# Kernel tuning notes

Measured on AMD Instinct MI355X. Metric: run time of the kernel, lower is better.

Reference implementation:

```python
import jax, jax.numpy as jnp
from jax import lax
import numpy as np

B, L = 256, 4096
H, RL, RH = 128, 2, 32   # num_hiddens, residual layers, residual hiddens
K, D = 512, 64           # codebook size, embedding dim
CC = 0.25                # commitment cost


def conv1d(x, w, b=None, stride=1, pad=0, circular=False):
    # x: (N,C,L), w: (O,I,k)
    if circular and pad > 0:
        x = jnp.pad(x, ((0, 0), (0, 0), (pad, pad)), mode='wrap')
        pad = 0
    y = lax.conv_general_dilated(x, w, (stride,), [(pad, pad)],
                                 dimension_numbers=('NCH', 'OIH', 'NCH'))
    return y if b is None else y + b[None, :, None]


def convt1d(x, w, b):
    # PyTorch ConvTranspose1d(k=4, s=2, p=1); w: (I,O,4). out_len = 2*L.
    wt = jnp.flip(jnp.swapaxes(w, 0, 1), -1)  # (O,I,4)
    y = lax.conv_general_dilated(x, wt, (1,), [(2, 2)], lhs_dilation=(2,),
                                 dimension_numbers=('NCH', 'OIH', 'NCH'))
    return y + b[None, :, None]


def res_stack(x, w1s, w2s):
    for i in range(w1s.shape[0]):
        h = conv1d(jax.nn.relu(x), w1s[i], None, 1, 1, circular=True)
        h = conv1d(jax.nn.relu(h), w2s[i], None, 1, 0)
        x = x + h
    return jax.nn.relu(x)


def setup_inputs() -> dict:
    key = jax.random.key(0)
    ks = iter(jax.random.split(key, 64))

    def w(*shape):
        fan_in = int(np.prod(shape[1:]))
        return jax.random.normal(next(ks), shape, jnp.float32) / np.sqrt(fan_in)

    def bias(n):
        return jax.random.uniform(next(ks), (n,), jnp.float32, -0.05, 0.05)

    inp = {'x': jax.random.normal(next(ks), (B, 1, L), jnp.float32)}
    # Encoder
    inp['enc_c1_w'] = w(H // 2, 1, 4);      inp['enc_c1_b'] = bias(H // 2)
    inp['enc_c2_w'] = w(H, H // 2, 4);      inp['enc_c2_b'] = bias(H)
    inp['enc_c3_w'] = w(H, H, 4);           inp['enc_c3_b'] = bias(H)
    inp['enc_c4_w'] = w(H, H, 4);           inp['enc_c4_b'] = bias(H)
    inp['enc_cf_w'] = w(H, H, 3);           inp['enc_cf_b'] = bias(H)
    inp['enc_res_w1'] = w(RL, RH, H, 3)
    inp['enc_res_w2'] = w(RL, H, RH, 1)
    # pre-VQ 1x1 conv
    inp['prevq_w'] = w(D, H, 1);            inp['prevq_b'] = bias(D)
    # codebook: uniform(-1/K, 1/K) as in source
    inp['emb'] = jax.random.uniform(next(ks), (K, D), jnp.float32, -1.0 / K, 1.0 / K)
    # Decoder
    inp['dec_init_w'] = w(H, D, 3);         inp['dec_init_b'] = bias(H)
    inp['dec_res_w1'] = w(RL, RH, H, 3)
    inp['dec_res_w2'] = w(RL, H, RH, 1)
    inp['ct0_w'] = w(H, H, 4);              inp['ct0_b'] = bias(H)
    inp['ct1_w'] = w(H, H, 4);              inp['ct1_b'] = bias(H)
    inp['ct2_w'] = w(H, H // 2, 4);         inp['ct2_b'] = bias(H // 2)
    inp['ct3_w'] = w(H // 2, 1, 4);         inp['ct3_b'] = bias(1)
    return inp


def _forward(x, enc_c1_w, enc_c1_b, enc_c2_w, enc_c2_b, enc_c3_w, enc_c3_b,
             enc_c4_w, enc_c4_b, enc_cf_w, enc_cf_b, enc_res_w1, enc_res_w2,
             prevq_w, prevq_b, emb, dec_init_w, dec_init_b, dec_res_w1,
             dec_res_w2, ct0_w, ct0_b, ct1_w, ct1_b, ct2_w, ct2_b, ct3_w, ct3_b):
    sg = lax.stop_gradient
    relu = jax.nn.relu
    # ---- Encoder (circular padding) ----
    z = relu(conv1d(x, enc_c1_w, enc_c1_b, 2, 1, circular=True))
    z = relu(conv1d(z, enc_c2_w, enc_c2_b, 2, 1, circular=True))
    z = relu(conv1d(z, enc_c3_w, enc_c3_b, 2, 1, circular=True))
    z = relu(conv1d(z, enc_c4_w, enc_c4_b, 2, 1, circular=True))
    z = conv1d(z, enc_cf_w, enc_cf_b, 1, 1, circular=True)
    z = res_stack(z, enc_res_w1, enc_res_w2)
    z = conv1d(z, prevq_w, prevq_b, 1, 0)        # (B, D, T)
    # ---- Vector quantizer ----
    z_t = jnp.transpose(z, (0, 2, 1))            # (B, T, D)
    flat = z_t.reshape(-1, D)                    # (BT, D)
    dist = (jnp.sum(flat ** 2, axis=1, keepdims=True)
            + jnp.sum(emb ** 2, axis=1)
            - 2.0 * flat @ emb.T)                # (BT, K)
    idx = jnp.argmin(dist, axis=1)               # (BT,)
    enc = jax.nn.one_hot(idx, K, dtype=flat.dtype)
    q = (enc @ emb).reshape(z_t.shape)           # (B, T, D)
    e_loss = jnp.mean((sg(q) - z_t) ** 2)
    q_loss = jnp.mean((q - sg(z_t)) ** 2)
    loss = q_loss + CC * e_loss
    q_st = z_t + sg(q - z_t)                     # straight-through
    avg = jnp.mean(enc, axis=0)
    perplexity = jnp.exp(-jnp.sum(avg * jnp.log(avg + 1e-10)))
    quantized = jnp.transpose(q_st, (0, 2, 1))   # (B, D, T)
    # ---- Decoder ----
    h = conv1d(quantized, dec_init_w, dec_init_b, 1, 1)
    h = res_stack(h, dec_res_w1, dec_res_w2)
    h = relu(convt1d(h, ct0_w, ct0_b))
    h = relu(convt1d(h, ct1_w, ct1_b))
    h = relu(convt1d(h, ct2_w, ct2_b))
    x_recon = convt1d(h, ct3_w, ct3_b)           # (B, 1, L)
    return loss, x_recon, perplexity


def reference(x, enc_c1_w, enc_c1_b, enc_c2_w, enc_c2_b, enc_c3_w, enc_c3_b,
              enc_c4_w, enc_c4_b, enc_cf_w, enc_cf_b, enc_res_w1, enc_res_w2,
              prevq_w, prevq_b, emb, dec_init_w, dec_init_b, dec_res_w1,
              dec_res_w2, ct0_w, ct0_b, ct1_w, ct1_b, ct2_w, ct2_b, ct3_w, ct3_b):
    return _forward(x, enc_c1_w, enc_c1_b, enc_c2_w, enc_c2_b, enc_c3_w,
                    enc_c3_b, enc_c4_w, enc_c4_b, enc_cf_w, enc_cf_b,
                    enc_res_w1, enc_res_w2, prevq_w, prevq_b, emb,
                    dec_init_w, dec_init_b, dec_res_w1, dec_res_w2,
                    ct0_w, ct0_b, ct1_w, ct1_b, ct2_w, ct2_b, ct3_w, ct3_b)
```

## Files before the change

### kernel.cpp

```cpp
#include <hip/hip_runtime.h>

#define DEVI __device__ __forceinline__

typedef __bf16 bf16x8 __attribute__((ext_vector_type(8)));
typedef float f32x4 __attribute__((ext_vector_type(4)));

DEVI ushort f2b(float f) {
  uint b = __float_as_uint(f);
  uint r = (b + 0x7FFFu + ((b >> 16) & 1u)) >> 16;
  return (ushort)r;
}
DEVI float b2f(ushort u) { return __uint_as_float(((uint)u) << 16); }

struct PrepArgs {
  int nw;
  int tot[20];
  const float* src[20];
  ushort* dst[20];
  int ci[20], co[20], sco[20], sci[20], sk[20];
};

__global__ __launch_bounds__(256)
void prep_all(PrepArgs a, int total) {
  int i = blockIdx.x * 256 + threadIdx.x;
  if (i >= total) return;
  int w = 0;
  while (i >= a.tot[w]) { i -= a.tot[w]; ++w; }
  const int li = i;
  const int CI = a.ci[w];
  int ciX = i % CI;
  int rest = i / CI;
  int coX = rest % a.co[w];
  int k = rest / a.co[w];
  a.dst[w][li] = f2b(a.src[w][coX * a.sco[w] + ciX * a.sci[w] + k * a.sk[w]]);
}

__global__ __launch_bounds__(256)
void enc1_bf(const float* __restrict__ x, const float* __restrict__ w1,
             const float* __restrict__ b1, ushort* __restrict__ out) {
  int i = blockIdx.x * 256 + threadIdx.x;
  int t = i & 2047, n = i >> 11;
  const float* xb = x + ((size_t)n << 12);
  int p = 2 * t - 1;
  float x0 = xb[(p + 4096) & 4095];
  float x1 = xb[(p + 4097) & 4095];
  float x2 = xb[(p + 4098) & 4095];
  float x3 = xb[(p + 4099) & 4095];
  uint ow[32];
  #pragma unroll
  for (int c2 = 0; c2 < 32; ++c2) {
    float4 wa = *reinterpret_cast<const float4*>(w1 + 8 * c2);
    float4 wb = *reinterpret_cast<const float4*>(w1 + 8 * c2 + 4);
    float s0 = fmaf(wa.x, x0, fmaf(wa.y, x1, fmaf(wa.z, x2, fmaf(wa.w, x3, b1[2 * c2]))));
    float s1 = fmaf(wb.x, x0, fmaf(wb.y, x1, fmaf(wb.z, x2, fmaf(wb.w, x3, b1[2 * c2 + 1]))));
    ow[c2] = (uint)f2b(fmaxf(s0, 0.0f)) | ((uint)f2b(fmaxf(s1, 0.0f)) << 16);
  }
  uint4* op = reinterpret_cast<uint4*>(out + ((size_t)i << 6));
  #pragma unroll
  for (int q = 0; q < 8; ++q)
    op[q] = uint4{ow[4 * q], ow[4 * q + 1], ow[4 * q + 2], ow[4 * q + 3]};
}

template<int CI, int CO, int K, int S, bool CIRC, bool GATHER>
__global__ __launch_bounds__(256)
void conv_mfma(const ushort* __restrict__ in, const ushort* __restrict__ wb,
               const float* __restrict__ bias, const ushort* __restrict__ resid,
               ushort* __restrict__ out, const int* __restrict__ gidx,
               int Tin, int in_relu, int out_relu) {
  constexpr int PAD = (K > 1) ? 1 : 0;
  constexpr int NT = 4;
  constexpr int TT = NT * 16;
  constexpr int SPAN = S * (TT - 1) + K;
  constexpr int CIG = CI / 8;
  constexpr int COT = CO / 16;
  constexpr int WCOT = (COT + 3) / 4;
  constexpr int WAVES_CO = COT / WCOT;
  constexpr int WAVES_T = 4 / WAVES_CO;
  constexpr int WTT = NT / WAVES_T;
  static_assert(CI % 32 == 0, "");

  __shared__ __align__(16) ushort xs[SPAN * CI];

  const int Tout = Tin / S;
  const int tilesPerB = Tout / TT;
  const int n = blockIdx.x / tilesPerB;
  const int t0 = (blockIdx.x % tilesPerB) * TT;
  const int tid = threadIdx.x;
  const int wid = tid >> 6, lane = tid & 63;
  const int l15 = lane & 15, l4 = lane >> 4;

  const int t_in0 = S * t0 - PAD;
  const ushort* inb = GATHER ? in : in + (size_t)n * Tin * CI;
  for (int i = tid; i < SPAN * CIG; i += 256) {
    int t = i / CIG, g = i - (i / CIG) * CIG;
    int tg = t_in0 + t;
    uint4 v;
    if (CIRC) {
      tg = (tg < 0) ? tg + Tin : (tg >= Tin ? tg - Tin : tg);
      v = *reinterpret_cast<const uint4*>(inb + (size_t)tg * CI + g * 8);
    } else if (GATHER) {
      if ((unsigned)tg < (unsigned)Tin) {
        int id = gidx[n * Tin + tg];
        v = *reinterpret_cast<const uint4*>(inb + (size_t)id * CI + g * 8);
      } else
        v = uint4{0, 0, 0, 0};
    } else {
      if ((unsigned)tg < (unsigned)Tin)
        v = *reinterpret_cast<const uint4*>(inb + (size_t)tg * CI + g * 8);
      else
        v = uint4{0, 0, 0, 0};
    }
    if (in_relu) {
      ushort* pv = reinterpret_cast<ushort*>(&v);
      #pragma unroll
      for (int e = 0; e < 8; ++e) pv[e] = (pv[e] & 0x8000) ? 0 : pv[e];
    }
    *reinterpret_cast<uint4*>(&xs[t * CI + ((g ^ (t & (CIG - 1))) * 8)]) = v;
  }
  __syncthreads();

  const int wco = wid % WAVES_CO;
  const int wt = wid / WAVES_CO;
  const int co_base = wco * WCOT * 16;
  const int t_base = wt * WTT * 16;

  f32x4 acc[WTT][WCOT] = {};

  for (int cc = 0; cc < CI / 32; ++cc) {
    #pragma unroll
    for (int k = 0; k < K; ++k) {
      bf16x8 bfr[WCOT];
      #pragma unroll
      for (int c = 0; c < WCOT; ++c) {
        const ushort* wp = wb + (size_t)((k * CO + co_base + c * 16 + l15)) * CI + cc * 32 + l4 * 8;
        bfr[c] = __builtin_bit_cast(bf16x8, *reinterpret_cast<const uint4*>(wp));
      }
      #pragma unroll
      for (int tt2 = 0; tt2 < WTT; ++tt2) {
        int trow = S * (t_base + tt2 * 16 + l15) + k;
        int g = cc * 4 + l4;
        bf16x8 afr = __builtin_bit_cast(bf16x8, *reinterpret_cast<const uint4*>(
            &xs[trow * CI + ((g ^ (trow & (CIG - 1))) * 8)]));
        #pragma unroll
        for (int c = 0; c < WCOT; ++c)
          acc[tt2][c] = __builtin_amdgcn_mfma_f32_16x16x32_bf16(afr, bfr[c], acc[tt2][c], 0, 0, 0);
      }
    }
  }

  float bv[WCOT];
  #pragma unroll
  for (int c = 0; c < WCOT; ++c)
    bv[c] = bias ? bias[co_base + c * 16 + l15] : 0.0f;
  ushort* outb = out + (size_t)n * Tout * CO;
  const ushort* resb = resid ? resid + (size_t)n * Tout * CO : nullptr;
  #pragma unroll
  for (int tt2 = 0; tt2 < WTT; ++tt2)
    #pragma unroll
    for (int c = 0; c < WCOT; ++c)
      #pragma unroll
      for (int r = 0; r < 4; ++r) {
        int t = t0 + t_base + tt2 * 16 + 4 * l4 + r;
        int co = co_base + c * 16 + l15;
        float v = acc[tt2][c][r] + bv[c];
        if (resb) v += b2f(resb[(size_t)t * CO + co]);
        if (out_relu) v = fmaxf(v, 0.0f);
        outb[(size_t)t * CO + co] = f2b(v);
      }
}

__global__ __launch_bounds__(256)
void res_mfma(const ushort* __restrict__ in, const ushort* __restrict__ wb1,
              const ushort* __restrict__ wb2, ushort* __restrict__ out) {
  constexpr int CI = 128, CIG = 16;
  constexpr int TT = 64, SPAN = 66, Tin = 256;
  __shared__ __align__(16) ushort xs[SPAN * CI];
  __shared__ __align__(16) ushort hs[TT][40];
  const int n = blockIdx.x >> 2;
  const int t0 = (blockIdx.x & 3) * TT;
  const int tid = threadIdx.x;
  const int wid = tid >> 6, lane = tid & 63;
  const int l15 = lane & 15, l4 = lane >> 4;
  const int t_in0 = t0 - 1;
  const ushort* inb = in + (size_t)n * Tin * CI;

  for (int i = tid; i < SPAN * CIG; i += 256) {
    int t = i >> 4, g = i & 15;
    int tg = t_in0 + t;
    tg = (tg < 0) ? tg + Tin : (tg >= Tin ? tg - Tin : tg);
    uint4 v = *reinterpret_cast<const uint4*>(inb + (size_t)tg * CI + g * 8);
    ushort* pv = reinterpret_cast<ushort*>(&v);
    #pragma unroll
    for (int e = 0; e < 8; ++e) pv[e] = (pv[e] & 0x8000) ? 0 : pv[e];
    *reinterpret_cast<uint4*>(&xs[t * CI + ((g ^ (t & 15)) * 8)]) = v;
  }
  __syncthreads();

  {
    f32x4 acc[2] = {};
    for (int cc = 0; cc < 4; ++cc)
      #pragma unroll
      for (int k = 0; k < 3; ++k) {
        bf16x8 bfr[2];
        #pragma unroll
        for (int c = 0; c < 2; ++c)
          bfr[c] = __builtin_bit_cast(bf16x8, *reinterpret_cast<const uint4*>(
              wb1 + (size_t)((k * 32 + c * 16 + l15)) * CI + cc * 32 + l4 * 8));
        int trow = wid * 16 + l15 + k;
        int g = cc * 4 + l4;
        bf16x8 afr = __builtin_bit_cast(bf16x8, *reinterpret_cast<const uint4*>(
            &xs[trow * CI + ((g ^ (trow & 15)) * 8)]));
        acc[0] = __builtin_amdgcn_mfma_f32_16x16x32_bf16(afr, bfr[0], acc[0], 0, 0, 0);
        acc[1] = __builtin_amdgcn_mfma_f32_16x16x32_bf16(afr, bfr[1], acc[1], 0, 0, 0);
      }
    #pragma unroll
    for (int c = 0; c < 2; ++c)
      #pragma unroll
      for (int r = 0; r < 4; ++r) {
        float v = acc[c][r];
        hs[wid * 16 + l4 * 4 + r][c * 16 + l15] = (v > 0.0f) ? f2b(v) : (ushort)0;
      }
  }
  __syncthreads();

  {
    bf16x8 afr = *reinterpret_cast<const bf16x8*>(&hs[wid * 16 + l15][l4 * 8]);
    f32x4 acc[8];
    #pragma unroll
    for (int c = 0; c < 8; ++c) {
      bf16x8 bfr = __builtin_bit_cast(bf16x8, *reinterpret_cast<const uint4*>(
          wb2 + (size_t)(c * 16 + l15) * 32 + l4 * 8));
      f32x4 z = {};
      acc[c] = __builtin_amdgcn_mfma_f32_16x16x32_bf16(afr, bfr, z, 0, 0, 0);
    }
    ushort* outb = out + (size_t)n * Tin * CI;
    #pragma unroll
    for (int c = 0; c < 8; ++c)
      #pragma unroll
      for (int r = 0; r < 4; ++r) {
        int t = t0 + wid * 16 + l4 * 4 + r;
        int co = c * 16 + l15;
        float v = acc[c][r] + b2f(inb[(size_t)t * CI + co]);
        outb[(size_t)t * CI + co] = f2b(v);
      }
  }
}

template<int CO>
__global__ __launch_bounds__(256)
void convt_mfma(const ushort* __restrict__ in, const ushort* __restrict__ wb,
                const float* __restrict__ bias, ushort* __restrict__ out,
                int Tin, int in_relu, int out_relu) {
  constexpr int CI = 128, CIG = 16;
  constexpr int NT = 4, TT = 64;
  constexpr int SPAN = TT + 2;
  constexpr int COT = CO / 16;
  constexpr int WCOT = (COT + 3) / 4;
  constexpr int WAVES_CO = COT / WCOT;
  constexpr int WTT = NT;

  __shared__ __align__(16) ushort xs[SPAN * CI];

  const int Tout = 2 * Tin;
  const int tilesPerB = Tin / TT;
  const int n = blockIdx.x / tilesPerB;
  const int tp0 = (blockIdx.x % tilesPerB) * TT;
  const int tid = threadIdx.x;
  const int wid = tid >> 6, lane = tid & 63;
  const int l15 = lane & 15, l4 = lane >> 4;

  const int t_in0 = tp0 - 1;
  const ushort* inb = in + (size_t)n * Tin * CI;
  for (int i = tid; i < SPAN * CIG; i += 256) {
    int t = i >> 4, g = i & 15;
    int tg = t_in0 + t;
    uint4 v;
    if ((unsigned)tg < (unsigned)Tin)
      v = *reinterpret_cast<const uint4*>(inb + (size_t)tg * CI + g * 8);
    else
      v = uint4{0, 0, 0, 0};
    if (in_relu) {
      ushort* pv = reinterpret_cast<ushort*>(&v);
      #pragma unroll
      for (int e = 0; e < 8; ++e) pv[e] = (pv[e] & 0x8000) ? 0 : pv[e];
    }
    *reinterpret_cast<uint4*>(&xs[t * CI + ((g ^ (t & 15)) * 8)]) = v;
  }
  __syncthreads();

  const int wco = wid % WAVES_CO;
  const int co_base = wco * WCOT * 16;

  f32x4 accE[WTT][WCOT] = {};
  f32x4 accO[WTT][WCOT] = {};

  for (int cc = 0; cc < 4; ++cc) {
    bf16x8 bk[4][WCOT];
    #pragma unroll
    for (int k = 0; k < 4; ++k)
      #pragma unroll
      for (int c = 0; c < WCOT; ++c) {
        const ushort* wp = wb + (size_t)((k * CO + co_base + c * 16 + l15)) * CI + cc * 32 + l4 * 8;
        bk[k][c] = __builtin_bit_cast(bf16x8, *reinterpret_cast<const uint4*>(wp));
      }
    #pragma unroll
    for (int tt2 = 0; tt2 < WTT; ++tt2) {
      int lt = tt2 * 16 + l15 + 1;
      int g = cc * 4 + l4;
      bf16x8 a0 = __builtin_bit_cast(bf16x8, *reinterpret_cast<const uint4*>(
          &xs[lt * CI + ((g ^ (lt & 15)) * 8)]));
      bf16x8 am = __builtin_bit_cast(bf16x8, *reinterpret_cast<const uint4*>(
          &xs[(lt - 1) * CI + ((g ^ ((lt - 1) & 15)) * 8)]));
      bf16x8 ap = __builtin_bit_cast(bf16x8, *reinterpret_cast<const uint4*>(
          &xs[(lt + 1) * CI + ((g ^ ((lt + 1) & 15)) * 8)]));
      #pragma unroll
      for (int c = 0; c < WCOT; ++c) {
        accE[tt2][c] = __builtin_amdgcn_mfma_f32_16x16x32_bf16(a0, bk[1][c], accE[tt2][c], 0, 0, 0);
        accE[tt2][c] = __builtin_amdgcn_mfma_f32_16x16x32_bf16(am, bk[3][c], accE[tt2][c], 0, 0, 0);
        accO[tt2][c] = __builtin_amdgcn_mfma_f32_16x16x32_bf16(ap, bk[0][c], accO[tt2][c], 0, 0, 0);
        accO[tt2][c] = __builtin_amdgcn_mfma_f32_16x16x32_bf16(a0, bk[2][c], accO[tt2][c], 0, 0, 0);
      }
    }
  }

  float bv[WCOT];
  #pragma unroll
  for (int c = 0; c < WCOT; ++c) bv[c] = bias[co_base + c * 16 + l15];
  ushort* outb = out + (size_t)n * Tout * CO;
  #pragma unroll
  for (int tt2 = 0; tt2 < WTT; ++tt2)
    #pragma unroll
    for (int c = 0; c < WCOT; ++c)
      #pragma unroll
      for (int r = 0; r < 4; ++r) {
        int tp = tp0 + tt2 * 16 + 4 * l4 + r;
        int co = co_base + c * 16 + l15;
        float vE = accE[tt2][c][r] + bv[c];
        float vO = accO[tt2][c][r] + bv[c];
        if (out_relu) { vE = fmaxf(vE, 0.0f); vO = fmaxf(vO, 0.0f); }
        outb[(size_t)(2 * tp) * CO + co] = f2b(vE);
        outb[(size_t)(2 * tp + 1) * CO + co] = f2b(vO);
      }
}

__global__ __launch_bounds__(256)
void ct3_bf(const ushort* __restrict__ in, const float* __restrict__ w3,
            const float* __restrict__ b3, float* __restrict__ out) {
  constexpr int SPAN = 130;
  __shared__ __align__(16) ushort ys[SPAN * 64];
  const int n = blockIdx.x >> 4;
  const int ot0 = (blockIdx.x & 15) << 8;
  const int tid = threadIdx.x;
  const int t_in0 = (ot0 >> 1) - 1;
  const ushort* inb = in + (size_t)n * 2048 * 64;
  for (int i = tid; i < SPAN * 8; i += 256) {
    int t = i >> 3, g = i & 7;
    int tg = t_in0 + t;
    uint4 v;
    if ((unsigned)tg < 2048u)
      v = *reinterpret_cast<const uint4*>(inb + (size_t)tg * 64 + g * 8);
    else
      v = uint4{0, 0, 0, 0};
    *reinterpret_cast<uint4*>(&ys[t * 64 + ((g ^ (t & 7)) * 8)]) = v;
  }
  __syncthreads();
  const int ot = ot0 + tid;
  const int odd = ot & 1;
  const int it_a = odd ? ((ot + 1) >> 1) : (ot >> 1);
  const int it_b = odd ? ((ot - 1) >> 1) : (ot / 2 - 1);
  const int ka = odd ? 0 : 1;
  const int kb = odd ? 2 : 3;
  const int lt_a = it_a - t_in0, lt_b = it_b - t_in0;
  float s = b3[0];
  #pragma unroll
  for (int g = 0; g < 8; ++g) {
    uint4 va = *reinterpret_cast<const uint4*>(&ys[lt_a * 64 + ((g ^ (lt_a & 7)) * 8)]);
    uint4 vb = *reinterpret_cast<const uint4*>(&ys[lt_b * 64 + ((g ^ (lt_b & 7)) * 8)]);
    const ushort* pa = reinterpret_cast<const ushort*>(&va);
    const ushort* pb = reinterpret_cast<const ushort*>(&vb);
    #pragma unroll
    for (int e = 0; e < 8; ++e) {
      int ci = g * 8 + e;
      s = fmaf(w3[ci * 4 + ka], b2f(pa[e]), s);
      s = fmaf(w3[ci * 4 + kb], b2f(pb[e]), s);
    }
  }
  out[(size_t)n * 4096 + ot] = s;
}

__global__ void ee_kernel(const float* __restrict__ emb, float* __restrict__ ee) {
  int c = blockIdx.x * 256 + threadIdx.x;
  if (c >= 512) return;
  float s = 0.0f;
  #pragma unroll
  for (int d = 0; d < 64; ++d) { float v = emb[c * 64 + d]; s = fmaf(v, v, s); }
  ee[c] = s;
}

__global__ __launch_bounds__(256)
void vq_mfma(const ushort* __restrict__ zt, const ushort* __restrict__ embb,
             const float* __restrict__ ee, int* __restrict__ idx,
             int* __restrict__ hist, float* __restrict__ loss_accum) {
  __shared__ __align__(16) ushort es[512 * 64];
  __shared__ float eel[512];
  __shared__ int lhist[512];
  const int tid = threadIdx.x;
  const int wid = tid >> 6, lane = tid & 63;
  const int l15 = lane & 15, l4 = lane >> 4;

  for (int i = tid; i < 512 * 8; i += 256) {
    int c = i >> 3, g = i & 7;
    reinterpret_cast<uint4*>(es)[c * 8 + (g ^ (c & 7))] =
        reinterpret_cast<const uint4*>(embb)[i];
  }
  for (int i = tid; i < 512; i += 256) { eel[i] = ee[i]; lhist[i] = 0; }
  __syncthreads();

  const int rb = blockIdx.x * 256 + wid * 64;
  bf16x8 bz[4][2];
  float zz[4], best[4];
  int bi[4];
  #pragma unroll
  for (int rt = 0; rt < 4; ++rt) {
    const int r = rb + rt * 16 + l15;
    uint4 v0 = *reinterpret_cast<const uint4*>(zt + (size_t)r * 64 + l4 * 8);
    uint4 v1 = *reinterpret_cast<const uint4*>(zt + (size_t)r * 64 + 32 + l4 * 8);
    bz[rt][0] = __builtin_bit_cast(bf16x8, v0);
    bz[rt][1] = __builtin_bit_cast(bf16x8, v1);
    float s = 0.0f;
    const ushort* p0 = reinterpret_cast<const ushort*>(&v0);
    const ushort* p1 = reinterpret_cast<const ushort*>(&v1);
    #pragma unroll
    for (int e = 0; e < 8; ++e) {
      float f0 = b2f(p0[e]), f1 = b2f(p1[e]);
      s = fmaf(f0, f0, fmaf(f1, f1, s));
    }
    s += __shfl_xor(s, 16);
    s += __shfl_xor(s, 32);
    zz[rt] = s;
    best[rt] = 3.4e38f;
    bi[rt] = 0;
  }

  for (int ct = 0; ct < 32; ++ct) {
    const int c = ct * 16 + l15;
    bf16x8 a0 = __builtin_bit_cast(bf16x8, reinterpret_cast<const uint4*>(es)[
        c * 8 + (l4 ^ (c & 7))]);
    bf16x8 a1 = __builtin_bit_cast(bf16x8, reinterpret_cast<const uint4*>(es)[
        c * 8 + ((4 | l4) ^ (c & 7))]);
    #pragma unroll
    for (int rt = 0; rt < 4; ++rt) {
      f32x4 acc = {};
      acc = __builtin_amdgcn_mfma_f32_16x16x32_bf16(a0, bz[rt][0], acc, 0, 0, 0);
      acc = __builtin_amdgcn_mfma_f32_16x16x32_bf16(a1, bz[rt][1], acc, 0, 0, 0);
      #pragma unroll
      for (int rr = 0; rr < 4; ++rr) {
        int code = ct * 16 + l4 * 4 + rr;
        float d = eel[code] - 2.0f * acc[rr];
        if (d < best[rt] || (d == best[rt] && code < bi[rt])) { best[rt] = d; bi[rt] = code; }
      }
    }
  }
  float vsum = 0.0f;
  #pragma unroll
  for (int rt = 0; rt < 4; ++rt) {
    #pragma unroll
    for (int m = 16; m <= 32; m <<= 1) {
      float ob = __shfl_xor(best[rt], m);
      int oi = __shfl_xor(bi[rt], m);
      if (ob < best[rt] || (ob == best[rt] && oi < bi[rt])) { best[rt] = ob; bi[rt] = oi; }
    }
    if (l4 == 0) {
      idx[rb + rt * 16 + l15] = bi[rt];
      atomicAdd(&lhist[bi[rt]], 1);
      vsum += zz[rt] + best[rt];
    }
  }
  #pragma unroll
  for (int m = 1; m < 64; m <<= 1) vsum += __shfl_xor(vsum, m);
  if (lane == 0) atomicAdd(loss_accum, vsum);
  __syncthreads();
  for (int i = tid; i < 512; i += 256)
    if (lhist[i]) atomicAdd(&hist[i], lhist[i]);
}

__global__ __launch_bounds__(512)
void finalize(const int* __restrict__ hist, const float* __restrict__ loss_accum,
              float* __restrict__ out) {
  __shared__ float red[8];
  int tid = threadIdx.x;
  float avg = (float)hist[tid] * (1.0f / 65536.0f);
  float v = avg * logf(avg + 1e-10f);
  for (int off = 32; off > 0; off >>= 1) v += __shfl_down(v, off);
  if ((tid & 63) == 0) red[tid >> 6] = v;
  __syncthreads();
  if (tid == 0) {
    float s = 0.0f;
    for (int i = 0; i < 8; ++i) s += red[i];
    out[1048577] = expf(-s);
    out[0] = 1.25f * loss_accum[0] * (1.0f / (65536.0f * 64.0f));
  }
}

extern "C" void kernel_launch(void* const* d_in, const int* in_sizes, int n_in,
                              void* d_out, int out_size, void* d_ws, size_t ws_size,
                              hipStream_t stream) {
  (void)in_sizes; (void)n_in; (void)out_size; (void)ws_size;
  const float* x    = (const float*)d_in[0];
  const float* c1w  = (const float*)d_in[1];
  const float* c1b  = (const float*)d_in[2];
  const float* c2w  = (const float*)d_in[3];
  const float* c2b  = (const float*)d_in[4];
  const float* c3w  = (const float*)d_in[5];
  const float* c3b  = (const float*)d_in[6];
  const float* c4w  = (const float*)d_in[7];
  const float* c4b  = (const float*)d_in[8];
  const float* cfw  = (const float*)d_in[9];
  const float* cfb  = (const float*)d_in[10];
  const float* erw1 = (const float*)d_in[11];
  const float* erw2 = (const float*)d_in[12];
  const float* pqw  = (const float*)d_in[13];
  const float* pqb  = (const float*)d_in[14];
  const float* emb  = (const float*)d_in[15];
  const float* diw  = (const float*)d_in[16];
  const float* dib  = (const float*)d_in[17];
  const float* drw1 = (const float*)d_in[18];
  const float* drw2 = (const float*)d_in[19];
  const float* t0w  = (const float*)d_in[20];
  const float* t0b  = (const float*)d_in[21];
  const float* t1w  = (const float*)d_in[22];
  const float* t1b  = (const float*)d_in[23];
  const float* t2w  = (const float*)d_in[24];
  const float* t2b  = (const float*)d_in[25];
  const float* t3w  = (const float*)d_in[26];
  const float* t3b  = (const float*)d_in[27];

  char* wsb = (char*)d_ws;
  ushort* R0 = (ushort*)wsb;
  ushort* R1 = (ushort*)(wsb + 67108864);
  ushort* R2 = (ushort*)(wsb + 134217728);
  ushort* R3 = (ushort*)(wsb + 0);
  ushort* R4 = (ushort*)(wsb + 16777216);
  ushort* R6 = (ushort*)(wsb + 37748736);
  ushort* WPu = (ushort*)(wsb + 167772160);
  ushort* wb_e2 = WPu + 0;
  ushort* wb_e3 = WPu + 32768;
  ushort* wb_e4 = WPu + 98304;
  ushort* wb_cf = WPu + 163840;
  ushort* wb_r1a = WPu + 212992;
  ushort* wb_r1b = WPu + 225280;
  ushort* wb_r2a = WPu + 237568;
  ushort* wb_r2b = WPu + 241664;
  ushort* wb_pq = WPu + 245760;
  ushort* wb_di = WPu + 253952;
  ushort* wb_d1a = WPu + 278528;
  ushort* wb_d1b = WPu + 290816;
  ushort* wb_d2a = WPu + 303104;
  ushort* wb_d2b = WPu + 307200;
  ushort* wb_t0 = WPu + 311296;
  ushort* wb_t1 = WPu + 376832;
  ushort* wb_t2 = WPu + 442368;
  ushort* wb_emb = WPu + 475136;
  char* fp = wsb + 167772160 + 1048576;
  float* eeb   = (float*)fp;
  int*   idxb  = (int*)(fp + 2048);
  int*   histb = (int*)(fp + 2048 + 262144);
  float* lossb = (float*)(fp + 2048 + 262144 + 2048);
  float* outp  = (float*)d_out;

  hipMemsetAsync(histb, 0, 512 * sizeof(int), stream);
  hipMemsetAsync(lossb, 0, sizeof(float), stream);

  PrepArgs pa{};
  int nw = 0, total = 0;
  auto addw = [&](const float* src, ushort* dst, int CO, int CI, int K,
                  int sco, int sci, int sk) {
    pa.tot[nw] = K * CO * CI; pa.src[nw] = src; pa.dst[nw] = dst;
    pa.ci[nw] = CI; pa.co[nw] = CO; pa.sco[nw] = sco; pa.sci[nw] = sci; pa.sk[nw] = sk;
    total += pa.tot[nw]; ++nw;
  };
  addw(c2w, wb_e2, 128, 64, 4, 256, 4, 1);
  addw(c3w, wb_e3, 128, 128, 4, 512, 4, 1);
  addw(c4w, wb_e4, 128, 128, 4, 512, 4, 1);
  addw(cfw, wb_cf, 128, 128, 3, 384, 3, 1);
  addw(erw1, wb_r1a, 32, 128, 3, 384, 3, 1);
  addw(erw1 + 12288, wb_r1b, 32, 128, 3, 384, 3, 1);
  addw(erw2, wb_r2a, 128, 32, 1, 32, 1, 1);
  addw(erw2 + 4096, wb_r2b, 128, 32, 1, 32, 1, 1);
  addw(pqw, wb_pq, 64, 128, 1, 128, 1, 1);
  addw(diw, wb_di, 128, 64, 3, 192, 3, 1);
  addw(drw1, wb_d1a, 32, 128, 3, 384, 3, 1);
  addw(drw1 + 12288, wb_d1b, 32, 128, 3, 384, 3, 1);
  addw(drw2, wb_d2a, 128, 32, 1, 32, 1, 1);
  addw(drw2 + 4096, wb_d2b, 128, 32, 1, 32, 1, 1);
  addw(t0w, wb_t0, 128, 128, 4, 4, 512, 1);
  addw(t1w, wb_t1, 128, 128, 4, 4, 512, 1);
  addw(t2w, wb_t2, 64, 128, 4, 4, 256, 1);
  addw(emb, wb_emb, 512, 64, 1, 64, 1, 1);
  pa.nw = nw;
  prep_all<<<(total + 255) / 256, 256, 0, stream>>>(pa, total);
  ee_kernel<<<2, 256, 0, stream>>>(emb, eeb);

  enc1_bf<<<2048, 256, 0, stream>>>(x, c1w, c1b, R0);
  conv_mfma<64, 128, 4, 2, true, false><<<4096, 256, 0, stream>>>(R0, wb_e2, c2b, nullptr, R1, nullptr, 2048, 0, 1);
  conv_mfma<128, 128, 4, 2, true, false><<<2048, 256, 0, stream>>>(R1, wb_e3, c3b, nullptr, R2, nullptr, 1024, 0, 1);
  conv_mfma<128, 128, 4, 2, true, false><<<1024, 256, 0, stream>>>(R2, wb_e4, c4b, nullptr, R3, nullptr, 512, 0, 1);
  conv_mfma<128, 128, 3, 1, true, false><<<1024, 256, 0, stream>>>(R3, wb_cf, cfb, nullptr, R4, nullptr, 256, 0, 0);
  res_mfma<<<1024, 256, 0, stream>>>(R4, wb_r1a, wb_r2a, R3);
  res_mfma<<<1024, 256, 0, stream>>>(R3, wb_r1b, wb_r2b, R4);
  conv_mfma<128, 64, 1, 1, false, false><<<1024, 256, 0, stream>>>(R4, wb_pq, pqb, nullptr, R6, nullptr, 256, 1, 0);
  vq_mfma<<<256, 256, 0, stream>>>(R6, wb_emb, eeb, idxb, histb, lossb);
  finalize<<<1, 512, 0, stream>>>(histb, lossb, outp);
  conv_mfma<64, 128, 3, 1, false, true><<<1024, 256, 0, stream>>>(wb_emb, wb_di, dib, nullptr, R3, idxb, 256, 0, 0);
  res_mfma<<<1024, 256, 0, stream>>>(R3, wb_d1a, wb_d2a, R4);
  res_mfma<<<1024, 256, 0, stream>>>(R4, wb_d1b, wb_d2b, R3);
  convt_mfma<128><<<1024, 256, 0, stream>>>(R3, wb_t0, t0b, R2, 256, 1, 1);
  convt_mfma<128><<<2048, 256, 0, stream>>>(R2, wb_t1, t1b, R0, 512, 0, 1);
  convt_mfma<64><<<4096, 256, 0, stream>>>(R0, wb_t2, t2b, R1, 1024, 0, 1);
  ct3_bf<<<4096, 256, 0, stream>>>(R1, t3w, t3b, outp + 1);
}
```

Measured before the change: 463.6 us.

## Fuse enc conv1 into conv2 and convT2 into convT3, retune tile shapes

Encoder conv1 (1→64 channels) is now computed on the fly in shared memory inside a new MFMA conv2 kernel, so the large 64-channel bf16 intermediate is never written to or read from HBM. In the same way, the last two transposed convolutions are fused: the convT2 output tile stays in LDS, including halo rows computed by extra MFMAs, and feeds the scalar convT3 directly. conv_mfma gains NT and WAVES_CO template parameters so the stride-1 layers use larger time tiles with half the blocks. It also hoists all K weight fragments per channel chunk and uses a stride-aware LDS swizzle to cut bank conflicts. The trade-offs are redundant recomputation of halo rows and higher register and LDS use per block.

```diff
diff --git a/kernel.cpp b/kernel.cpp
--- a/kernel.cpp
+++ b/kernel.cpp
@@ -35,49 +35,22 @@
   a.dst[w][li] = f2b(a.src[w][coX * a.sco[w] + ciX * a.sci[w] + k * a.sk[w]]);
 }
 
-__global__ __launch_bounds__(256)
-void enc1_bf(const float* __restrict__ x, const float* __restrict__ w1,
-             const float* __restrict__ b1, ushort* __restrict__ out) {
-  int i = blockIdx.x * 256 + threadIdx.x;
-  int t = i & 2047, n = i >> 11;
-  const float* xb = x + ((size_t)n << 12);
-  int p = 2 * t - 1;
-  float x0 = xb[(p + 4096) & 4095];
-  float x1 = xb[(p + 4097) & 4095];
-  float x2 = xb[(p + 4098) & 4095];
-  float x3 = xb[(p + 4099) & 4095];
-  uint ow[32];
-  #pragma unroll
-  for (int c2 = 0; c2 < 32; ++c2) {
-    float4 wa = *reinterpret_cast<const float4*>(w1 + 8 * c2);
-    float4 wb = *reinterpret_cast<const float4*>(w1 + 8 * c2 + 4);
-    float s0 = fmaf(wa.x, x0, fmaf(wa.y, x1, fmaf(wa.z, x2, fmaf(wa.w, x3, b1[2 * c2]))));
-    float s1 = fmaf(wb.x, x0, fmaf(wb.y, x1, fmaf(wb.z, x2, fmaf(wb.w, x3, b1[2 * c2 + 1]))));
-    ow[c2] = (uint)f2b(fmaxf(s0, 0.0f)) | ((uint)f2b(fmaxf(s1, 0.0f)) << 16);
-  }
-  uint4* op = reinterpret_cast<uint4*>(out + ((size_t)i << 6));
-  #pragma unroll
-  for (int q = 0; q < 8; ++q)
-    op[q] = uint4{ow[4 * q], ow[4 * q + 1], ow[4 * q + 2], ow[4 * q + 3]};
-}
-
-template<int CI, int CO, int K, int S, bool CIRC, bool GATHER>
+template<int CI, int CO, int K, int S, bool CIRC, bool GATHER, int NT, int WAVES_CO>
 __global__ __launch_bounds__(256)
 void conv_mfma(const ushort* __restrict__ in, const ushort* __restrict__ wb,
                const float* __restrict__ bias, const ushort* __restrict__ resid,
                ushort* __restrict__ out, const int* __restrict__ gidx,
                int Tin, int in_relu, int out_relu) {
   constexpr int PAD = (K > 1) ? 1 : 0;
-  constexpr int NT = 4;
   constexpr int TT = NT * 16;
   constexpr int SPAN = S * (TT - 1) + K;
   constexpr int CIG = CI / 8;
   constexpr int COT = CO / 16;
-  constexpr int WCOT = (COT + 3) / 4;
-  constexpr int WAVES_CO = COT / WCOT;
+  constexpr int WCOT = COT / WAVES_CO;
   constexpr int WAVES_T = 4 / WAVES_CO;
   constexpr int WTT = NT / WAVES_T;
-  static_assert(CI % 32 == 0, "");
+  constexpr int KSH = (S == 2) ? 1 : 0;
+  static_assert(CI % 32 == 0 && COT % WAVES_CO == 0 && NT % WAVES_T == 0, "");
 
   __shared__ __align__(16) ushort xs[SPAN * CI];
 
@@ -115,7 +88,7 @@
       #pragma unroll
       for (int e = 0; e < 8; ++e) pv[e] = (pv[e] & 0x8000) ? 0 : pv[e];
     }
-    *reinterpret_cast<uint4*>(&xs[t * CI + ((g ^ (t & (CIG - 1))) * 8)]) = v;
+    *reinterpret_cast<uint4*>(&xs[t * CI + ((g ^ ((t >> KSH) & (CIG - 1))) * 8)]) = v;
   }
   __syncthreads();
 
@@ -127,23 +100,24 @@
   f32x4 acc[WTT][WCOT] = {};
 
   for (int cc = 0; cc < CI / 32; ++cc) {
+    bf16x8 bk[K][WCOT];
+    #pragma unroll
+    for (int k = 0; k < K; ++k)
+      #pragma unroll
+      for (int c = 0; c < WCOT; ++c)
+        bk[k][c] = __builtin_bit_cast(bf16x8, *reinterpret_cast<const uint4*>(
+            wb + (size_t)((k * CO + co_base + c * 16 + l15)) * CI + cc * 32 + l4 * 8));
     #pragma unroll
     for (int k = 0; k < K; ++k) {
-      bf16x8 bfr[WCOT];
-      #pragma unroll
-      for (int c = 0; c < WCOT; ++c) {
-        const ushort* wp = wb + (size_t)((k * CO + co_base + c * 16 + l15)) * CI + cc * 32 + l4 * 8;
-        bfr[c] = __builtin_bit_cast(bf16x8, *reinterpret_cast<const uint4*>(wp));
-      }
       #pragma unroll
       for (int tt2 = 0; tt2 < WTT; ++tt2) {
         int trow = S * (t_base + tt2 * 16 + l15) + k;
         int g = cc * 4 + l4;
         bf16x8 afr = __builtin_bit_cast(bf16x8, *reinterpret_cast<const uint4*>(
-            &xs[trow * CI + ((g ^ (trow & (CIG - 1))) * 8)]));
+            &xs[trow * CI + ((g ^ ((trow >> KSH) & (CIG - 1))) * 8)]));
         #pragma unroll
         for (int c = 0; c < WCOT; ++c)
-          acc[tt2][c] = __builtin_amdgcn_mfma_f32_16x16x32_bf16(afr, bfr[c], acc[tt2][c], 0, 0, 0);
+          acc[tt2][c] = __builtin_amdgcn_mfma_f32_16x16x32_bf16(afr, bk[k][c], acc[tt2][c], 0, 0, 0);
       }
     }
   }
@@ -166,6 +140,91 @@
         if (resb) v += b2f(resb[(size_t)t * CO + co]);
         if (out_relu) v = fmaxf(v, 0.0f);
         outb[(size_t)t * CO + co] = f2b(v);
+      }
+}
+
+__global__ __launch_bounds__(256)
+void enc12_mfma(const float* __restrict__ x, const float* __restrict__ w1,
+                const float* __restrict__ b1, const ushort* __restrict__ wb,
+                const float* __restrict__ b2, ushort* __restrict__ out) {
+  constexpr int CI = 64, CO = 128, K = 4, NT = 8;
+  constexpr int TT = 128, SPAN = 2 * 127 + 4;
+  constexpr int CIG = 8, WCOT = 4, WTT = 4;
+  __shared__ __align__(16) ushort xs[SPAN * CI];
+  __shared__ float xl[520];
+
+  const int n = blockIdx.x >> 3;
+  const int t0 = (blockIdx.x & 7) * TT;
+  const int tid = threadIdx.x;
+  const int wid = tid >> 6, lane = tid & 63;
+  const int l15 = lane & 15, l4 = lane >> 4;
+  const int t_in0 = 2 * t0 - 1;
+  const int xw0 = 2 * t_in0 - 1;
+  const float* xb = x + ((size_t)n << 12);
+
+  for (int j = tid; j < 518; j += 256)
+    xl[j] = xb[(xw0 + j + 8192) & 4095];
+  __syncthreads();
+
+  for (int i = tid; i < SPAN * CIG; i += 256) {
+    int t = i >> 3, g = i & 7;
+    float xv0 = xl[2 * t], xv1 = xl[2 * t + 1], xv2 = xl[2 * t + 2], xv3 = xl[2 * t + 3];
+    uint pack[4];
+    #pragma unroll
+    for (int h = 0; h < 4; ++h) {
+      int c0 = g * 8 + 2 * h;
+      float4 wa = *reinterpret_cast<const float4*>(w1 + 4 * c0);
+      float4 wc = *reinterpret_cast<const float4*>(w1 + 4 * c0 + 4);
+      float s0 = fmaf(wa.x, xv0, fmaf(wa.y, xv1, fmaf(wa.z, xv2, fmaf(wa.w, xv3, b1[c0]))));
+      float s1 = fmaf(wc.x, xv0, fmaf(wc.y, xv1, fmaf(wc.z, xv2, fmaf(wc.w, xv3, b1[c0 + 1]))));
+      pack[h] = (uint)f2b(fmaxf(s0, 0.0f)) | ((uint)f2b(fmaxf(s1, 0.0f)) << 16);
+    }
+    *reinterpret_cast<uint4*>(&xs[t * CI + ((g ^ ((t >> 1) & 7)) * 8)]) =
+        uint4{pack[0], pack[1], pack[2], pack[3]};
+  }
+  __syncthreads();
+
+  const int wco = wid & 1;
+  const int wt = wid >> 1;
+  const int co_base = wco * 64;
+  const int t_base = wt * 64;
+
+  f32x4 acc[WTT][WCOT] = {};
+  for (int cc = 0; cc < 2; ++cc) {
+    bf16x8 bk[K][WCOT];
+    #pragma unroll
+    for (int k = 0; k < K; ++k)
+      #pragma unroll
+      for (int c = 0; c < WCOT; ++c)
+        bk[k][c] = __builtin_bit_cast(bf16x8, *reinterpret_cast<const uint4*>(
+            wb + (size_t)((k * CO + co_base + c * 16 + l15)) * CI + cc * 32 + l4 * 8));
+    #pragma unroll
+    for (int k = 0; k < K; ++k) {
+      #pragma unroll
+      for (int tt2 = 0; tt2 < WTT; ++tt2) {
+        int trow = 2 * (t_base + tt2 * 16 + l15) + k;
+        int g = cc * 4 + l4;
+        bf16x8 afr = __builtin_bit_cast(bf16x8, *reinterpret_cast<const uint4*>(
+            &xs[trow * CI + ((g ^ ((trow >> 1) & 7)) * 8)]));
+        #pragma unroll
+        for (int c = 0; c < WCOT; ++c)
+          acc[tt2][c] = __builtin_amdgcn_mfma_f32_16x16x32_bf16(afr, bk[k][c], acc[tt2][c], 0, 0, 0);
+      }
+    }
+  }
+  float bv[WCOT];
+  #pragma unroll
+  for (int c = 0; c < WCOT; ++c) bv[c] = b2[co_base + c * 16 + l15];
+  ushort* outb = out + (size_t)n * 1024 * CO;
+  #pragma unroll
+  for (int tt2 = 0; tt2 < WTT; ++tt2)
+    #pragma unroll
+    for (int c = 0; c < WCOT; ++c)
+      #pragma unroll
+      for (int r = 0; r < 4; ++r) {
+        int t = t0 + t_base + tt2 * 16 + 4 * l4 + r;
+        int co = co_base + c * 16 + l15;
+        outb[(size_t)t * CO + co] = f2b(fmaxf(acc[tt2][c][r] + bv[c], 0.0f));
       }
 }
 
@@ -299,10 +358,9 @@
     #pragma unroll
     for (int k = 0; k < 4; ++k)
       #pragma unroll
-      for (int c = 0; c < WCOT; ++c) {
-        const ushort* wp = wb + (size_t)((k * CO + co_base + c * 16 + l15)) * CI + cc * 32 + l4 * 8;
-        bk[k][c] = __builtin_bit_cast(bf16x8, *reinterpret_cast<const uint4*>(wp));
-      }
+      for (int c = 0; c < WCOT; ++c)
+        bk[k][c] = __builtin_bit_cast(bf16x8, *reinterpret_cast<const uint4*>(
+            wb + (size_t)((k * CO + co_base + c * 16 + l15)) * CI + cc * 32 + l4 * 8));
     #pragma unroll
     for (int tt2 = 0; tt2 < WTT; ++tt2) {
       int lt = tt2 * 16 + l15 + 1;
@@ -344,38 +402,98 @@
 }
 
 __global__ __launch_bounds__(256)
-void ct3_bf(const ushort* __restrict__ in, const float* __restrict__ w3,
-            const float* __restrict__ b3, float* __restrict__ out) {
-  constexpr int SPAN = 130;
-  __shared__ __align__(16) ushort ys[SPAN * 64];
+void ct23_mfma(const ushort* __restrict__ in, const ushort* __restrict__ wb,
+               const float* __restrict__ bias, const float* __restrict__ w3,
+               const float* __restrict__ b3, float* __restrict__ out) {
+  constexpr int CI = 128, CO = 64, CIG = 16;
+  constexpr int TT = 64, SPAN = 66, Tin = 1024;
+  __shared__ __align__(16) ushort xs[SPAN * CI];
+  __shared__ __align__(16) ushort ys[130 * 64];
+
   const int n = blockIdx.x >> 4;
-  const int ot0 = (blockIdx.x & 15) << 8;
+  const int tp0 = (blockIdx.x & 15) * TT;
   const int tid = threadIdx.x;
-  const int t_in0 = (ot0 >> 1) - 1;
-  const ushort* inb = in + (size_t)n * 2048 * 64;
-  for (int i = tid; i < SPAN * 8; i += 256) {
-    int t = i >> 3, g = i & 7;
+  const int wid = tid >> 6, lane = tid & 63;
+  const int l15 = lane & 15, l4 = lane >> 4;
+  const int t_in0 = tp0 - 1;
+  const ushort* inb = in + (size_t)n * Tin * CI;
+
+  for (int i = tid; i < SPAN * CIG; i += 256) {
+    int t = i >> 4, g = i & 15;
     int tg = t_in0 + t;
     uint4 v;
-    if ((unsigned)tg < 2048u)
-      v = *reinterpret_cast<const uint4*>(inb + (size_t)tg * 64 + g * 8);
+    if ((unsigned)tg < (unsigned)Tin)
+      v = *reinterpret_cast<const uint4*>(inb + (size_t)tg * CI + g * 8);
     else
       v = uint4{0, 0, 0, 0};
-    *reinterpret_cast<uint4*>(&ys[t * 64 + ((g ^ (t & 7)) * 8)]) = v;
-  }
-  __syncthreads();
-  const int ot = ot0 + tid;
-  const int odd = ot & 1;
-  const int it_a = odd ? ((ot + 1) >> 1) : (ot >> 1);
-  const int it_b = odd ? ((ot - 1) >> 1) : (ot / 2 - 1);
+    *reinterpret_cast<uint4*>(&xs[t * CI + ((g ^ (t & 15)) * 8)]) = v;
+  }
+  __syncthreads();
+
+  const int co_base = wid * 16;
+  f32x4 accE[4] = {}, accO[4] = {};
+  f32x4 hO = {}, hE = {};
+
+  for (int cc = 0; cc < 4; ++cc) {
+    bf16x8 bk[4];
+    #pragma unroll
+    for (int k = 0; k < 4; ++k)
+      bk[k] = __builtin_bit_cast(bf16x8, *reinterpret_cast<const uint4*>(
+          wb + (size_t)((k * CO + co_base + l15)) * CI + cc * 32 + l4 * 8));
+    const int g = cc * 4 + l4;
+    auto rd = [&](int lt) -> bf16x8 {
+      return __builtin_bit_cast(bf16x8, *reinterpret_cast<const uint4*>(
+          &xs[lt * CI + ((g ^ (lt & 15)) * 8)]));
+    };
+    #pragma unroll
+    for (int tt2 = 0; tt2 < 4; ++tt2) {
+      int lt = tt2 * 16 + l15 + 1;
+      bf16x8 a0 = rd(lt), am = rd(lt - 1), ap = rd(lt + 1);
+      accE[tt2] = __builtin_amdgcn_mfma_f32_16x16x32_bf16(a0, bk[1], accE[tt2], 0, 0, 0);
+      accE[tt2] = __builtin_amdgcn_mfma_f32_16x16x32_bf16(am, bk[3], accE[tt2], 0, 0, 0);
+      accO[tt2] = __builtin_amdgcn_mfma_f32_16x16x32_bf16(ap, bk[0], accO[tt2], 0, 0, 0);
+      accO[tt2] = __builtin_amdgcn_mfma_f32_16x16x32_bf16(a0, bk[2], accO[tt2], 0, 0, 0);
+    }
+    bf16x8 h0 = rd(0), h1 = rd(1), h64 = rd(64), h65 = rd(65);
+    hO = __builtin_amdgcn_mfma_f32_16x16x32_bf16(h1, bk[0], hO, 0, 0, 0);
+    hO = __builtin_amdgcn_mfma_f32_16x16x32_bf16(h0, bk[2], hO, 0, 0, 0);
+    hE = __builtin_amdgcn_mfma_f32_16x16x32_bf16(h65, bk[1], hE, 0, 0, 0);
+    hE = __builtin_amdgcn_mfma_f32_16x16x32_bf16(h64, bk[3], hE, 0, 0, 0);
+  }
+
+  const float bv = bias[co_base + l15];
+  auto ywr = [&](int j, int co, float v) {
+    int g = co >> 3, e = co & 7;
+    ys[j * 64 + ((g ^ (j & 7)) * 8) + e] = f2b(fmaxf(v, 0.0f));
+  };
+  #pragma unroll
+  for (int tt2 = 0; tt2 < 4; ++tt2)
+    #pragma unroll
+    for (int r = 0; r < 4; ++r) {
+      int m = tt2 * 16 + 4 * l4 + r;
+      ywr(2 * m + 1, co_base + l15, accE[tt2][r] + bv);
+      ywr(2 * m + 2, co_base + l15, accO[tt2][r] + bv);
+    }
+  if (l4 == 0) {
+    float vO = (tp0 == 0) ? -1.0f : hO[0] + bv;
+    float vE = (tp0 + TT == Tin) ? -1.0f : hE[0] + bv;
+    ywr(0, co_base + l15, vO);
+    ywr(129, co_base + l15, vE);
+  }
+  __syncthreads();
+
+  const int o = 4 * tp0 + tid;
+  const int odd = o & 1;
+  const int ga = odd ? ((o + 1) >> 1) : (o >> 1);
+  const int gb = odd ? ((o - 1) >> 1) : (o / 2 - 1);
   const int ka = odd ? 0 : 1;
   const int kb = odd ? 2 : 3;
-  const int lt_a = it_a - t_in0, lt_b = it_b - t_in0;
+  const int la = ga - (2 * tp0 - 1), lb = gb - (2 * tp0 - 1);
   float s = b3[0];
   #pragma unroll
   for (int g = 0; g < 8; ++g) {
-    uint4 va = *reinterpret_cast<const uint4*>(&ys[lt_a * 64 + ((g ^ (lt_a & 7)) * 8)]);
-    uint4 vb = *reinterpret_cast<const uint4*>(&ys[lt_b * 64 + ((g ^ (lt_b & 7)) * 8)]);
+    uint4 va = *reinterpret_cast<const uint4*>(&ys[la * 64 + ((g ^ (la & 7)) * 8)]);
+    uint4 vb = *reinterpret_cast<const uint4*>(&ys[lb * 64 + ((g ^ (lb & 7)) * 8)]);
     const ushort* pa = reinterpret_cast<const ushort*>(&va);
     const ushort* pb = reinterpret_cast<const ushort*>(&vb);
     #pragma unroll
@@ -385,7 +503,7 @@
       s = fmaf(w3[ci * 4 + kb], b2f(pb[e]), s);
     }
   }
-  out[(size_t)n * 4096 + ot] = s;
+  out[(size_t)n * 4096 + o] = s;
 }
 
 __global__ void ee_kernel(const float* __restrict__ emb, float* __restrict__ ee) {
@@ -601,21 +719,19 @@
   prep_all<<<(total + 255) / 256, 256, 0, stream>>>(pa, total);
   ee_kernel<<<2, 256, 0, stream>>>(emb, eeb);
 
-  enc1_bf<<<2048, 256, 0, stream>>>(x, c1w, c1b, R0);
-  conv_mfma<64, 128, 4, 2, true, false><<<4096, 256, 0, stream>>>(R0, wb_e2, c2b, nullptr, R1, nullptr, 2048, 0, 1);
-  conv_mfma<128, 128, 4, 2, true, false><<<2048, 256, 0, stream>>>(R1, wb_e3, c3b, nullptr, R2, nullptr, 1024, 0, 1);
-  conv_mfma<128, 128, 4, 2, true, false><<<1024, 256, 0, stream>>>(R2, wb_e4, c4b, nullptr, R3, nullptr, 512, 0, 1);
-  conv_mfma<128, 128, 3, 1, true, false><<<1024, 256, 0, stream>>>(R3, wb_cf, cfb, nullptr, R4, nullptr, 256, 0, 0);
+  enc12_mfma<<<2048, 256, 0, stream>>>(x, c1w, c1b, wb_e2, c2b, R1);
+  conv_mfma<128, 128, 4, 2, true, false, 4, 4><<<2048, 256, 0, stream>>>(R1, wb_e3, c3b, nullptr, R2, nullptr, 1024, 0, 1);
+  conv_mfma<128, 128, 4, 2, true, false, 4, 4><<<1024, 256, 0, stream>>>(R2, wb_e4, c4b, nullptr, R3, nullptr, 512, 0, 1);
+  conv_mfma<128, 128, 3, 1, true, false, 8, 2><<<512, 256, 0, stream>>>(R3, wb_cf, cfb, nullptr, R4, nullptr, 256, 0, 0);
   res_mfma<<<1024, 256, 0, stream>>>(R4, wb_r1a, wb_r2a, R3);
   res_mfma<<<1024, 256, 0, stream>>>(R3, wb_r1b, wb_r2b, R4);
-  conv_mfma<128, 64, 1, 1, false, false><<<1024, 256, 0, stream>>>(R4, wb_pq, pqb, nullptr, R6, nullptr, 256, 1, 0);
+  conv_mfma<128, 64, 1, 1, false, false, 8, 2><<<512, 256, 0, stream>>>(R4, wb_pq, pqb, nullptr, R6, nullptr, 256, 1, 0);
   vq_mfma<<<256, 256, 0, stream>>>(R6, wb_emb, eeb, idxb, histb, lossb);
   finalize<<<1, 512, 0, stream>>>(histb, lossb, outp);
-  conv_mfma<64, 128, 3, 1, false, true><<<1024, 256, 0, stream>>>(wb_emb, wb_di, dib, nullptr, R3, idxb, 256, 0, 0);
+  conv_mfma<64, 128, 3, 1, false, true, 8, 2><<<512, 256, 0, stream>>>(wb_emb, wb_di, dib, nullptr, R3, idxb, 256, 0, 0);
   res_mfma<<<1024, 256, 0, stream>>>(R3, wb_d1a, wb_d2a, R4);
   res_mfma<<<1024, 256, 0, stream>>>(R4, wb_d1b, wb_d2b, R3);
   convt_mfma<128><<<1024, 256, 0, stream>>>(R3, wb_t0, t0b, R2, 256, 1, 1);
   convt_mfma<128><<<2048, 256, 0, stream>>>(R2, wb_t1, t1b, R0, 512, 0, 1);
-  convt_mfma<64><<<4096, 256, 0, stream>>>(R0, wb_t2, t2b, R1, 1024, 0, 1);
-  ct3_bf<<<4096, 256, 0, stream>>>(R1, t3w, t3b, outp + 1);
-}
+  ct23_mfma<<<4096, 256, 0, stream>>>(R0, wb_t2, t2b, t3w, t3b, outp + 1);
+}
```

Measured after the change: 478.5 us. 1.03x slower.
